# Optimization experiments

Hardware: AMD Instinct MI355X
Metric: run time of the kernel (lower is better)

Reference implementation:

```python
import jax, jax.numpy as jnp
import numpy as np

B, S, D, H, F, M, DC = 2, 1024, 1024, 16, 4096, 2048, 256
HD = D // H

def rmsnorm(x, w, eps=1e-6):
    return x * jax.lax.rsqrt(jnp.mean(x * x, axis=-1, keepdims=True) + eps) * w

def setup_inputs() -> dict:
    key = jax.random.key(0)
    ks = jax.random.split(key, 16)
    def w(i, shape):
        return jax.random.normal(ks[i], shape, jnp.float32) * (1.0 / np.sqrt(shape[0]))
    # real RoPE tables
    inv = 1.0 / (10000.0 ** (jnp.arange(0, HD, 2, dtype=jnp.float32) / HD))
    freqs = jnp.outer(jnp.arange(S, dtype=jnp.float32), inv)
    emb = jnp.concatenate([freqs, freqs], axis=-1)  # [S, HD]
    return {
        "hidden_states": jax.random.normal(ks[0], (B, S, D), jnp.float32),
        "mem_keys": jnp.zeros((B, M, DC), jnp.float32),
        "mem_values": jnp.zeros((B, M, D), jnp.float32),
        "cos": jnp.cos(emb), "sin": jnp.sin(emb),
        "norm1_w": jnp.ones((D,), jnp.float32),
        "norm2_w": jnp.ones((D,), jnp.float32),
        "norm_mem_w": jnp.ones((D,), jnp.float32),
        "Wq": w(1, (D, D)), "Wk": w(2, (D, D)), "Wv": w(3, (D, D)), "Wo": w(4, (D, D)),
        "W_content": w(5, (D, D)), "W_comp": w(6, (D, DC)), "W_strength": w(7, (D, 1)),
        "W_query": w(8, (D, DC)),
        "W_gate": w(9, (2 * D, D)), "W_proj": w(10, (D, D)),
        "W1": w(11, (D, F)), "W3": w(12, (D, F)), "W2": w(13, (F, D)),
        "position": 0,
    }

def reference(hidden_states, mem_keys, mem_values, cos, sin,
              norm1_w, norm2_w, norm_mem_w,
              Wq, Wk, Wv, Wo,
              W_content, W_comp, W_strength, W_query,
              W_gate, W_proj, W1, W3, W2, position):
    b, s, d = hidden_states.shape
    h = hidden_states
    # 1) causal self-attention with RoPE
    n = rmsnorm(h, norm1_w)
    def heads(x):
        return x.reshape(b, s, H, HD).transpose(0, 2, 1, 3)  # [b,h,s,hd]
    q, k, v = heads(n @ Wq), heads(n @ Wk), heads(n @ Wv)
    def rot(x):
        x1, x2 = jnp.split(x, 2, axis=-1)
        return jnp.concatenate([-x2, x1], axis=-1)
    c, si = cos[None, None], sin[None, None]
    q = q * c + rot(q) * si
    k = k * c + rot(k) * si
    scores = jnp.einsum('bhqd,bhkd->bhqk', q, k) / np.sqrt(HD)
    causal = jnp.tril(jnp.ones((s, s), bool))
    scores = jnp.where(causal, scores, jnp.float32(-1e30))
    attn = jax.nn.softmax(scores, axis=-1)
    attn_out = jnp.einsum('bhqk,bhkd->bhqd', attn, v).transpose(0, 2, 1, 3).reshape(b, s, d) @ Wo
    h = h + attn_out
    # 2) memory snapshot write: the original per-token python loop writes each token
    #    to consecutive circular-buffer slots; with M >= s the slots are unique, so
    #    the loop vectorizes into a single scatter.
    content = h @ W_content                     # [b,s,d]
    compressed = h @ W_comp                     # [b,s,DC]
    strength = jax.nn.sigmoid(h @ W_strength)   # [b,s,1]
    idx = (position + jnp.arange(s)) % mem_keys.shape[1]
    old_k = mem_keys[:, idx]
    old_v = mem_values[:, idx]
    new_keys = mem_keys.at[:, idx].set(strength * compressed + (1.0 - strength) * old_k)
    new_values = mem_values.at[:, idx].set(strength * content + (1.0 - strength) * old_v)
    # 3) memory retrieval (attention over slots)
    normed = rmsnorm(h, norm_mem_w)
    qm = normed @ W_query                       # [b,s,DC]
    mscores = jnp.einsum('bsd,bmd->bsm', qm, new_keys) / np.sqrt(DC)
    mattn = jax.nn.softmax(mscores, axis=-1)
    retrieved = jnp.einsum('bsm,bmd->bsd', mattn, new_values)
    # 4) gated memory integration
    gate = jax.nn.sigmoid(jnp.concatenate([h, retrieved], axis=-1) @ W_gate)
    h = h + gate * (retrieved @ W_proj)
    # 5) SwiGLU FFN
    n2 = rmsnorm(h, norm2_w)
    h = h + (jax.nn.silu(n2 @ W1) * (n2 @ W3)) @ W2
    return (h, new_keys, new_values)
```

## Files before the change

### kernel.cpp

```cpp
#include <hip/hip_runtime.h>
#include <hip/hip_bf16.h>
#include <math.h>

typedef __bf16 bf16;
typedef __attribute__((ext_vector_type(8))) __bf16 bf16x8;
typedef __attribute__((ext_vector_type(4))) __bf16 bf16x4;
typedef __attribute__((ext_vector_type(4))) float f32x4;

#define B_ 2
#define S_ 1024
#define D_ 1024
#define H_ 16
#define HD_ 64
#define F_ 4096
#define M_ 2048
#define DC_ 256
#define NTOK (B_*S_)

__device__ __forceinline__ void gload16(const void* g, void* l) {
    __builtin_amdgcn_global_load_lds(
        (__attribute__((address_space(1))) void*)(void*)(g),
        (__attribute__((address_space(3))) void*)(l), 16, 0, 0);
}

template<int N> __device__ __forceinline__ void wait_vm() {
    if constexpr (N == 0)      asm volatile("s_waitcnt vmcnt(0)" ::: "memory");
    else if constexpr (N == 2) asm volatile("s_waitcnt vmcnt(2)" ::: "memory");
    else if constexpr (N == 4) asm volatile("s_waitcnt vmcnt(4)" ::: "memory");
    else if constexpr (N == 6) asm volatile("s_waitcnt vmcnt(6)" ::: "memory");
    else                       asm volatile("s_waitcnt vmcnt(8)" ::: "memory");
}
__device__ __forceinline__ void wait_lgkm0() {
    asm volatile("s_waitcnt lgkmcnt(0)" ::: "memory");
}

template<int BM, int BN, bool OUTBF>
__global__ __launch_bounds__(256) void mgemm(
    const bf16* __restrict__ A, const bf16* __restrict__ Bt,
    const float* __restrict__ resid, void* __restrict__ Cout,
    int K, int lda, int ldb, int ldc,
    long long sA, long long sB, long long sC)
{
    constexpr int WN   = (BM == 128) ? 2 : 4;
    constexpr int WCOL = BN / WN;
    constexpr int FN   = WCOL / 16;
    constexpr int LA = BM * 64, LB = BN * 64;
    constexpr int LPS = BM / 32 + BN / 32;
    __shared__ bf16 lds[2 * (LA + LB)];
    const int z = blockIdx.z;
    A  += (size_t)z * sA;
    Bt += (size_t)z * sB;
    const int gx = gridDim.x;
    const int nwg = gx * gridDim.y;
    const int flat = blockIdx.y * gx + blockIdx.x;
    const int q8 = nwg >> 3, r8 = nwg & 7;
    const int xcd = flat & 7, lid = flat >> 3;
    const int swz = (xcd < r8 ? xcd * (q8 + 1) : r8 * (q8 + 1) + (xcd - r8) * q8) + lid;
    const int band = swz / (8 * gx);
    const int rem  = swz % (8 * gx);
    const int row0 = (band * 8 + (rem & 7)) * BM;
    const int col0 = (rem >> 3) * BN;
    const int tid = threadIdx.x, wid = tid >> 6, lane = tid & 63;
    const int wr = wid / WN, wc = wid % WN;
    const int srow = lane >> 3;
    const int ssub = (lane & 7) ^ (srow & 7);

    f32x4 acc[4][FN];
    #pragma unroll
    for (int m = 0; m < 4; ++m)
        #pragma unroll
        for (int n = 0; n < FN; ++n) acc[m][n] = (f32x4){0.f, 0.f, 0.f, 0.f};

    auto STAGE = [&](int buf, int k0) {
        bf16* Ab = lds + buf * (LA + LB);
        bf16* Bb = Ab + LA;
        #pragma unroll
        for (int i = 0; i < BM / 32; ++i) {
            int c = wid * (BM / 32) + i;
            gload16(A + (size_t)(row0 + c * 8 + srow) * lda + k0 + ssub * 8, Ab + c * 512);
        }
        #pragma unroll
        for (int i = 0; i < BN / 32; ++i) {
            int c = wid * (BN / 32) + i;
            gload16(Bt + (size_t)(col0 + c * 8 + srow) * ldb + k0 + ssub * 8, Bb + c * 512);
        }
    };

    const int nt = K >> 6;
    STAGE(0, 0);
    if (nt > 1) STAGE(1, 64);
    for (int t = 0; t < nt; ++t) {
        if (t < nt - 1) wait_vm<LPS>();
        else            wait_vm<0>();
        __builtin_amdgcn_sched_barrier(0);
        __builtin_amdgcn_s_barrier();
        __builtin_amdgcn_sched_barrier(0);
        const bf16* Ab = lds + (t & 1) * (LA + LB);
        const bf16* Bb = Ab + LA;
        const int ar = wr * 64 + (lane & 15);
        const int br = wc * WCOL + (lane & 15);
        #pragma unroll
        for (int ksel = 0; ksel < 2; ++ksel) {
            const int ps = ((ksel << 2) + (lane >> 4)) ^ (lane & 7);
            bf16x8 af[4], bfr[FN];
            #pragma unroll
            for (int m = 0; m < 4; ++m)
                af[m] = *(const bf16x8*)(Ab + (ar + m * 16) * 64 + ps * 8);
            #pragma unroll
            for (int n = 0; n < FN; ++n)
                bfr[n] = *(const bf16x8*)(Bb + (br + n * 16) * 64 + ps * 8);
            #pragma unroll
            for (int m = 0; m < 4; ++m)
                #pragma unroll
                for (int n = 0; n < FN; ++n)
                    acc[m][n] = __builtin_amdgcn_mfma_f32_16x16x32_bf16(af[m], bfr[n], acc[m][n], 0, 0, 0);
        }
        wait_lgkm0();
        __builtin_amdgcn_sched_barrier(0);
        __builtin_amdgcn_s_barrier();
        __builtin_amdgcn_sched_barrier(0);
        if (t + 2 < nt) STAGE(t & 1, (t + 2) << 6);
    }
    const int crow = row0 + wr * 64 + ((lane >> 4) << 2);
    const int ccol = col0 + wc * WCOL + (lane & 15);
    #pragma unroll
    for (int m = 0; m < 4; ++m)
        #pragma unroll
        for (int n = 0; n < FN; ++n)
            #pragma unroll
            for (int r = 0; r < 4; ++r) {
                size_t idx = (size_t)(crow + m * 16 + r) * ldc + ccol + n * 16;
                float v = acc[m][n][r];
                if (resid) v += resid[idx];
                if (OUTBF) ((bf16*)Cout)[(size_t)z * sC + idx] = (bf16)v;
                else       ((float*)Cout)[(size_t)z * sC + idx] = v;
            }
}

__global__ __launch_bounds__(256) void flash_attn(
    const bf16* __restrict__ qkv, const bf16* __restrict__ vt,
    bf16* __restrict__ o)
{
    __shared__ bf16 qlds[64 * 64];
    __shared__ bf16 klds[2][64 * 64];
    __shared__ bf16 vlds[2][64 * 64];
    __shared__ bf16 plds[4][16 * 64];
    const int qt = blockIdx.x, hh = blockIdx.y, b = blockIdx.z;
    const int qb0 = qt * 64;
    const int tid = threadIdx.x, wid = tid >> 6, lane = tid & 63;
    const bf16* qg = qkv + (size_t)b * S_ * 3072 + hh * 64;
    const bf16* kg = qg + 1024;
    const bf16* vg = vt + (size_t)(b * H_ + hh) * 64 * 1024;
    const int srow = lane >> 3;
    const int ssub = (lane & 7) ^ (srow & 7);

    #pragma unroll
    for (int i = 0; i < 2; ++i) {
        int c = wid * 2 + i;
        gload16(qg + (size_t)(qb0 + c * 8 + srow) * 3072 + ssub * 8, qlds + c * 512);
    }
    auto STAGE = [&](int buf, int kb) {
        #pragma unroll
        for (int i = 0; i < 2; ++i) {
            int c = wid * 2 + i;
            gload16(kg + (size_t)(kb + c * 8 + srow) * 3072 + ssub * 8, klds[buf] + c * 512);
            gload16(vg + (size_t)(c * 8 + srow) * 1024 + kb + ssub * 8, vlds[buf] + c * 512);
        }
    };

    const int nt = qt + 1;
    STAGE(0, 0);
    if (nt > 1) STAGE(1, 64);

    f32x4 oacc[4];
    #pragma unroll
    for (int n = 0; n < 4; ++n) oacc[n] = (f32x4){0.f, 0.f, 0.f, 0.f};
    float mrow[4] = {-1e30f, -1e30f, -1e30f, -1e30f};
    float lrow[4] = {0.f, 0.f, 0.f, 0.f};
    bf16x8 qf[2];
    bf16* pw = plds[wid];
    const int qlr = (lane >> 4) * 4;

    for (int t = 0; t < nt; ++t) {
        if (t < nt - 1) wait_vm<4>();
        else            wait_vm<0>();
        __builtin_amdgcn_sched_barrier(0);
        __builtin_amdgcn_s_barrier();
        __builtin_amdgcn_sched_barrier(0);
        if (t == 0) {
            const int ar = wid * 16 + (lane & 15);
            #pragma unroll
            for (int ksel = 0; ksel < 2; ++ksel) {
                const int ps = ((ksel << 2) + (lane >> 4)) ^ (lane & 7);
                qf[ksel] = *(const bf16x8*)(qlds + ar * 64 + ps * 8);
            }
        }
        const bf16* Kb = klds[t & 1];
        const bf16* Vb = vlds[t & 1];
        f32x4 sacc[4];
        #pragma unroll
        for (int n = 0; n < 4; ++n) sacc[n] = (f32x4){0.f, 0.f, 0.f, 0.f};
        #pragma unroll
        for (int ksel = 0; ksel < 2; ++ksel) {
            const int ps = ((ksel << 2) + (lane >> 4)) ^ (lane & 7);
            #pragma unroll
            for (int n = 0; n < 4; ++n) {
                bf16x8 kf = *(const bf16x8*)(Kb + (n * 16 + (lane & 15)) * 64 + ps * 8);
                sacc[n] = __builtin_amdgcn_mfma_f32_16x16x32_bf16(qf[ksel], kf, sacc[n], 0, 0, 0);
            }
        }
        if (t == nt - 1) {
            const int qrow = qb0 + wid * 16 + qlr;
            const int kcol = t * 64 + (lane & 15);
            #pragma unroll
            for (int n = 0; n < 4; ++n)
                #pragma unroll
                for (int r = 0; r < 4; ++r)
                    if (kcol + n * 16 > qrow + r) sacc[n][r] = -1e30f;
        }
        #pragma unroll
        for (int r = 0; r < 4; ++r) {
            float mx = fmaxf(fmaxf(sacc[0][r], sacc[1][r]), fmaxf(sacc[2][r], sacc[3][r]));
            #pragma unroll
            for (int off = 8; off > 0; off >>= 1) mx = fmaxf(mx, __shfl_xor(mx, off));
            float mnew = fmaxf(mrow[r], mx);
            float scale = __expf(mrow[r] - mnew);
            float rs = 0.f;
            #pragma unroll
            for (int n = 0; n < 4; ++n) {
                float p = __expf(sacc[n][r] - mnew);
                sacc[n][r] = p;
                rs += p;
            }
            #pragma unroll
            for (int off = 8; off > 0; off >>= 1) rs += __shfl_xor(rs, off);
            lrow[r] = lrow[r] * scale + rs;
            mrow[r] = mnew;
            #pragma unroll
            for (int n = 0; n < 4; ++n) oacc[n][r] *= scale;
        }
        #pragma unroll
        for (int n = 0; n < 4; ++n)
            #pragma unroll
            for (int r = 0; r < 4; ++r) {
                const int qr = qlr + r;
                const int k = n * 16 + (lane & 15);
                const int su = (k >> 3) ^ (qr & 7);
                pw[qr * 64 + su * 8 + (k & 7)] = (bf16)sacc[n][r];
            }
        #pragma unroll
        for (int ksel = 0; ksel < 2; ++ksel) {
            const int ps = ((ksel << 2) + (lane >> 4)) ^ (lane & 7);
            bf16x8 pa = *(const bf16x8*)(pw + (lane & 15) * 64 + ps * 8);
            #pragma unroll
            for (int n = 0; n < 4; ++n) {
                bf16x8 vf = *(const bf16x8*)(Vb + (n * 16 + (lane & 15)) * 64 + ps * 8);
                oacc[n] = __builtin_amdgcn_mfma_f32_16x16x32_bf16(pa, vf, oacc[n], 0, 0, 0);
            }
        }
        wait_lgkm0();
        __builtin_amdgcn_sched_barrier(0);
        __builtin_amdgcn_s_barrier();
        __builtin_amdgcn_sched_barrier(0);
        if (t + 2 < nt) STAGE(t & 1, (t + 2) * 64);
    }
    float inv[4];
    #pragma unroll
    for (int r = 0; r < 4; ++r) inv[r] = 1.f / lrow[r];
    #pragma unroll
    for (int n = 0; n < 4; ++n)
        #pragma unroll
        for (int r = 0; r < 4; ++r) {
            const int q = qb0 + wid * 16 + qlr + r;
            const int d = n * 16 + (lane & 15);
            o[(size_t)(b * S_ + q) * 1024 + hh * 64 + d] = (bf16)(oacc[n][r] * inv[r]);
        }
}

template<typename TI>
__global__ __launch_bounds__(256) void tcast(
    const TI* __restrict__ in, bf16* __restrict__ out,
    int lin, int lout, long long sin, long long sout)
{
    __shared__ float t[32][33];
    in  += (size_t)blockIdx.z * sin;
    out += (size_t)blockIdx.z * sout;
    const int c0 = blockIdx.x * 32, r0 = blockIdx.y * 32;
    const int tx = threadIdx.x & 31, ty = threadIdx.x >> 5;
    #pragma unroll
    for (int j = 0; j < 4; ++j)
        t[ty + j * 8][tx] = (float)in[(size_t)(r0 + ty + j * 8) * lin + c0 + tx];
    __syncthreads();
    #pragma unroll
    for (int j = 0; j < 4; ++j)
        out[(size_t)(c0 + ty + j * 8) * lout + r0 + tx] = (bf16)t[tx][ty + j * 8];
}

__global__ __launch_bounds__(256) void rmsnorm_bf(
    const float* __restrict__ x, const float* __restrict__ w, bf16* __restrict__ out)
{
    __shared__ float red[4];
    const int row = blockIdx.x, tid = threadIdx.x;
    const float* xr = x + (size_t)row * D_;
    f32x4 v = *(const f32x4*)(xr + tid * 4);
    float ss = v.x * v.x + v.y * v.y + v.z * v.z + v.w * v.w;
    #pragma unroll
    for (int off = 32; off > 0; off >>= 1) ss += __shfl_xor(ss, off);
    if ((tid & 63) == 0) red[tid >> 6] = ss;
    __syncthreads();
    float scn = rsqrtf((red[0] + red[1] + red[2] + red[3]) * (1.f / D_) + 1e-6f);
    f32x4 wv = *(const f32x4*)(w + tid * 4);
    bf16x4 o;
    o[0] = (bf16)(v.x * scn * wv.x); o[1] = (bf16)(v.y * scn * wv.y);
    o[2] = (bf16)(v.z * scn * wv.z); o[3] = (bf16)(v.w * scn * wv.w);
    *(bf16x4*)(out + (size_t)row * D_ + tid * 4) = o;
}

__global__ void rope_kernel(bf16* __restrict__ qkv,
                            const float* __restrict__ cosp, const float* __restrict__ sinp)
{
    int idx = blockIdx.x * 256 + threadIdx.x;
    int p = idx & 31, hh = (idx >> 5) & 15, s = (idx >> 9) & 1023, b = idx >> 19;
    size_t base = ((size_t)(b * S_ + s)) * 3072 + hh * 64;
    float c1 = cosp[s * 64 + p],      s1 = sinp[s * 64 + p];
    float c2 = cosp[s * 64 + p + 32], s2 = sinp[s * 64 + p + 32];
    float q1 = (float)qkv[base + p], q2 = (float)qkv[base + p + 32];
    qkv[base + p]      = (bf16)((q1 * c1 - q2 * s1) * 0.125f);
    qkv[base + p + 32] = (bf16)((q2 * c2 + q1 * s2) * 0.125f);
    size_t kb = base + 1024;
    float k1 = (float)qkv[kb + p], k2 = (float)qkv[kb + p + 32];
    qkv[kb + p]      = (bf16)(k1 * c1 - k2 * s1);
    qkv[kb + p + 32] = (bf16)(k2 * c2 + k1 * s2);
}

__global__ __launch_bounds__(256) void mem_softmax(
    const float* __restrict__ ms, bf16* __restrict__ out)
{
    __shared__ float red[4];
    const int row = blockIdx.x, tid = threadIdx.x;
    const float* r = ms + (size_t)row * 2048;
    f32x4 a = *(const f32x4*)(r + tid * 8);
    f32x4 b = *(const f32x4*)(r + tid * 8 + 4);
    float xs[8] = {a.x, a.y, a.z, a.w, b.x, b.y, b.z, b.w};
    float mx = -1e30f;
    #pragma unroll
    for (int i = 0; i < 8; ++i) mx = fmaxf(mx, xs[i]);
    #pragma unroll
    for (int off = 32; off > 0; off >>= 1) mx = fmaxf(mx, __shfl_xor(mx, off));
    if ((tid & 63) == 0) red[tid >> 6] = mx;
    __syncthreads();
    mx = fmaxf(fmaxf(red[0], red[1]), fmaxf(red[2], red[3]));
    __syncthreads();
    float sum = 0.f;
    #pragma unroll
    for (int i = 0; i < 8; ++i) { xs[i] = __expf((xs[i] - mx) * 0.0625f); sum += xs[i]; }
    #pragma unroll
    for (int off = 32; off > 0; off >>= 1) sum += __shfl_xor(sum, off);
    if ((tid & 63) == 0) red[tid >> 6] = sum;
    __syncthreads();
    float inv = 1.f / (red[0] + red[1] + red[2] + red[3]);
    bf16x8 o;
    #pragma unroll
    for (int i = 0; i < 8; ++i) o[i] = (bf16)(xs[i] * inv);
    *(bf16x8*)(out + (size_t)row * 2048 + tid * 8) = o;
}

__global__ void strength_kernel(const float* __restrict__ h, const float* __restrict__ ws,
                                float* __restrict__ st)
{
    const int row = blockIdx.x, lane = threadIdx.x;
    const float* hr = h + (size_t)row * D_;
    float s = 0.f;
    #pragma unroll
    for (int it = 0; it < 4; ++it) {
        f32x4 hv = *(const f32x4*)(hr + it * 256 + lane * 4);
        f32x4 wv = *(const f32x4*)(ws + it * 256 + lane * 4);
        s += hv.x * wv.x + hv.y * wv.y + hv.z * wv.z + hv.w * wv.w;
    }
    #pragma unroll
    for (int off = 32; off > 0; off >>= 1) s += __shfl_xor(s, off);
    if (lane == 0) st[row] = 1.f / (1.f + expf(-s));
}

__global__ void scatter_keys_kernel(const float* __restrict__ ctcp, const float* __restrict__ st,
                                    const float* __restrict__ memk, const int* __restrict__ pos,
                                    float* __restrict__ outk)
{
    int idx = blockIdx.x * 256 + threadIdx.x;
    int c = (idx & 63) * 4;
    int s = (idx >> 6) & (S_ - 1);
    int b = idx >> 16;
    int row = (pos[0] + s) % M_;
    float t = st[b * S_ + s];
    size_t mi = ((size_t)b * M_ + row) * DC_ + c;
    f32x4 cv = *(const f32x4*)(ctcp + ((size_t)b * S_ + s) * 1280 + 1024 + c);
    f32x4 mv = *(const f32x4*)(memk + mi);
    f32x4 o = {t * cv.x + (1.f - t) * mv.x, t * cv.y + (1.f - t) * mv.y,
               t * cv.z + (1.f - t) * mv.z, t * cv.w + (1.f - t) * mv.w};
    *(f32x4*)(outk + mi) = o;
}

__global__ void scatter_vals_kernel(const float* __restrict__ ctcp, const float* __restrict__ st,
                                    const float* __restrict__ memv, const int* __restrict__ pos,
                                    float* __restrict__ outv)
{
    int idx = blockIdx.x * 256 + threadIdx.x;
    int c = (idx & 255) * 4;
    int s = (idx >> 8) & (S_ - 1);
    int b = idx >> 18;
    int row = (pos[0] + s) % M_;
    float t = st[b * S_ + s];
    size_t mi = ((size_t)b * M_ + row) * D_ + c;
    f32x4 cv = *(const f32x4*)(ctcp + ((size_t)b * S_ + s) * 1280 + c);
    f32x4 mv = *(const f32x4*)(memv + mi);
    f32x4 o = {t * cv.x + (1.f - t) * mv.x, t * cv.y + (1.f - t) * mv.y,
               t * cv.z + (1.f - t) * mv.z, t * cv.w + (1.f - t) * mv.w};
    *(f32x4*)(outv + mi) = o;
}

__global__ void cast_h1_kernel(const float* __restrict__ h1, bf16* __restrict__ cat)
{
    int i = blockIdx.x * 256 + threadIdx.x;
    int row = i >> 8, c = (i & 255) * 4;
    f32x4 v = *(const f32x4*)(h1 + (size_t)row * 1024 + c);
    bf16x4 o = {(bf16)v.x, (bf16)v.y, (bf16)v.z, (bf16)v.w};
    *(bf16x4*)(cat + (size_t)row * 2048 + c) = o;
}

__global__ void cast_flat_kernel(const float* __restrict__ in, bf16* __restrict__ out)
{
    int i = blockIdx.x * 256 + threadIdx.x;
    f32x4 v = *(const f32x4*)(in + (size_t)i * 4);
    bf16x4 o = {(bf16)v.x, (bf16)v.y, (bf16)v.z, (bf16)v.w};
    *(bf16x4*)(out + (size_t)i * 4) = o;
}

__global__ void gatecomb_kernel(const float* __restrict__ h1, const float* __restrict__ g,
                                const float* __restrict__ p, float* __restrict__ h2)
{
    int i = blockIdx.x * 256 + threadIdx.x;
    f32x4 hv = *(const f32x4*)(h1 + (size_t)i * 4);
    f32x4 gv = *(const f32x4*)(g + (size_t)i * 4);
    f32x4 pv = *(const f32x4*)(p + (size_t)i * 4);
    f32x4 o;
    o.x = hv.x + pv.x / (1.f + expf(-gv.x));
    o.y = hv.y + pv.y / (1.f + expf(-gv.y));
    o.z = hv.z + pv.z / (1.f + expf(-gv.z));
    o.w = hv.w + pv.w / (1.f + expf(-gv.w));
    *(f32x4*)(h2 + (size_t)i * 4) = o;
}

__global__ void silumul_kernel(const bf16* __restrict__ a13, bf16* __restrict__ a1bf)
{
    int i = blockIdx.x * 256 + threadIdx.x;
    int row = i >> 10, c = (i & 1023) * 4;
    bf16x4 xv = *(const bf16x4*)(a13 + (size_t)row * 8192 + c);
    bf16x4 yv = *(const bf16x4*)(a13 + (size_t)row * 8192 + 4096 + c);
    bf16x4 o;
    #pragma unroll
    for (int j = 0; j < 4; ++j) {
        float x = (float)xv[j];
        o[j] = (bf16)((x / (1.f + expf(-x))) * (float)yv[j]);
    }
    *(bf16x4*)(a1bf + (size_t)row * 4096 + c) = o;
}

extern "C" void kernel_launch(void* const* d_in, const int* in_sizes, int n_in,
                              void* d_out, int out_size, void* d_ws, size_t ws_size,
                              hipStream_t stream)
{
    const float* h0   = (const float*)d_in[0];
    const float* memk = (const float*)d_in[1];
    const float* memv = (const float*)d_in[2];
    const float* cosp = (const float*)d_in[3];
    const float* sinp = (const float*)d_in[4];
    const float* n1w  = (const float*)d_in[5];
    const float* n2w  = (const float*)d_in[6];
    const float* nmw  = (const float*)d_in[7];
    const float* Wq   = (const float*)d_in[8];
    const float* Wk   = (const float*)d_in[9];
    const float* Wv   = (const float*)d_in[10];
    const float* Wo   = (const float*)d_in[11];
    const float* Wct  = (const float*)d_in[12];
    const float* Wcp  = (const float*)d_in[13];
    const float* Wst  = (const float*)d_in[14];
    const float* Wqr  = (const float*)d_in[15];
    const float* Wg   = (const float*)d_in[16];
    const float* Wpj  = (const float*)d_in[17];
    const float* W1   = (const float*)d_in[18];
    const float* W3   = (const float*)d_in[19];
    const float* W2   = (const float*)d_in[20];
    const int*   pos  = (const int*)d_in[21];

    float* out_h = (float*)d_out;
    float* out_k = out_h + (size_t)NTOK * D_;
    float* out_v = out_k + (size_t)B_ * M_ * DC_;

    char* W = (char*)d_ws;
    const size_t MB = 1u << 20;
    bf16*  qkvb = (bf16*)(W);
    bf16*  vtb  = (bf16*)(W + 12 * MB);
    bf16*  nbf  = (bf16*)(W + 16 * MB);
    bf16*  abf  = (bf16*)(W + 20 * MB);
    float* h1b  = (float*)(W + 24 * MB);
    bf16*  catbf= (bf16*)(W + 32 * MB);
    float* ctcp = (float*)(W + 40 * MB);
    float* stb  = (float*)(W + 51 * MB);
    float* msb  = (float*)(W + 52 * MB);
    bf16*  matt = (bf16*)(W + 68 * MB);
    bf16*  nvt  = (bf16*)(W + 76 * MB);
    bf16*  a13  = (bf16*)(W + 52 * MB);
    bf16*  a1bf = (bf16*)(W);
    bf16*  okbf = (bf16*)(W + 84 * MB);
    bf16*  qmbf = (bf16*)(W + 86 * MB);
    float* aob  = (float*)(W + 88 * MB);
    float* h2b  = (float*)(W + 96 * MB);
    bf16*  WqkvT= (bf16*)(W + 104 * MB);
    bf16*  WoT  = (bf16*)(W + 110 * MB);
    bf16*  WctcpT=(bf16*)(W + 112 * MB);
    bf16*  WqrT = (bf16*)(W + 115 * MB);
    bf16*  WgT  = (bf16*)(W + 116 * MB);
    bf16*  WpjT = (bf16*)(W + 120 * MB);
    bf16*  W13T = (bf16*)(W + 122 * MB);
    bf16*  W2T  = (bf16*)(W + 138 * MB);

    tcast<float><<<dim3(32, 32, 1), 256, 0, stream>>>(Wq,  WqkvT,                1024, 1024, 0, 0);
    tcast<float><<<dim3(32, 32, 1), 256, 0, stream>>>(Wk,  WqkvT + 1024 * 1024,  1024, 1024, 0, 0);
    tcast<float><<<dim3(32, 32, 1), 256, 0, stream>>>(Wv,  WqkvT + 2048 * 1024,  1024, 1024, 0, 0);
    tcast<float><<<dim3(32, 32, 1), 256, 0, stream>>>(Wo,  WoT,                  1024, 1024, 0, 0);
    tcast<float><<<dim3(32, 32, 1), 256, 0, stream>>>(Wct, WctcpT,               1024, 1024, 0, 0);
    tcast<float><<<dim3(8, 32, 1), 256, 0, stream>>>(Wcp,  WctcpT + 1024 * 1024, 256, 1024, 0, 0);
    tcast<float><<<dim3(8, 32, 1), 256, 0, stream>>>(Wqr,  WqrT,                 256, 1024, 0, 0);
    tcast<float><<<dim3(32, 64, 1), 256, 0, stream>>>(Wg,  WgT,                  1024, 2048, 0, 0);
    tcast<float><<<dim3(32, 32, 1), 256, 0, stream>>>(Wpj, WpjT,                 1024, 1024, 0, 0);
    tcast<float><<<dim3(128, 32, 1), 256, 0, stream>>>(W1, W13T,                 4096, 1024, 0, 0);
    tcast<float><<<dim3(128, 32, 1), 256, 0, stream>>>(W3, W13T + 4096 * 1024,   4096, 1024, 0, 0);
    tcast<float><<<dim3(32, 128, 1), 256, 0, stream>>>(W2, W2T,                  1024, 4096, 0, 0);

    rmsnorm_bf<<<NTOK, 256, 0, stream>>>(h0, n1w, nbf);
    mgemm<64, 128, true><<<dim3(24, 32, 1), 256, 0, stream>>>(
        nbf, WqkvT, nullptr, qkvb, 1024, 1024, 1024, 3072, 0, 0, 0);
    rope_kernel<<<(B_ * S_ * H_ * 32) / 256, 256, 0, stream>>>(qkvb, cosp, sinp);
    for (int b = 0; b < B_; ++b)
        tcast<bf16><<<dim3(2, 32, 16), 256, 0, stream>>>(
            qkvb + (size_t)b * S_ * 3072 + 2048, vtb + (size_t)b * 16 * 65536,
            3072, 1024, 64, 65536);

    flash_attn<<<dim3(S_ / 64, H_, B_), 256, 0, stream>>>(qkvb, vtb, abf);

    mgemm<64, 64, false><<<dim3(16, 32, 1), 256, 0, stream>>>(
        abf, WoT, h0, h1b, 1024, 1024, 1024, 1024, 0, 0, 0);
    cast_h1_kernel<<<(NTOK * D_) / 1024, 256, 0, stream>>>(h1b, catbf);
    strength_kernel<<<NTOK, 64, 0, stream>>>(h1b, Wst, stb);

    mgemm<64, 64, false><<<dim3(20, 32, 1), 256, 0, stream>>>(
        catbf, WctcpT, nullptr, ctcp, 1024, 2048, 1024, 1280, 0, 0, 0);
    hipMemcpyAsync(out_k, memk, (size_t)B_ * M_ * DC_ * sizeof(float), hipMemcpyDeviceToDevice, stream);
    hipMemcpyAsync(out_v, memv, (size_t)B_ * M_ * D_ * sizeof(float), hipMemcpyDeviceToDevice, stream);
    scatter_keys_kernel<<<(B_ * S_ * DC_) / 1024, 256, 0, stream>>>(ctcp, stb, memk, pos, out_k);
    scatter_vals_kernel<<<(B_ * S_ * D_) / 1024, 256, 0, stream>>>(ctcp, stb, memv, pos, out_v);

    rmsnorm_bf<<<NTOK, 256, 0, stream>>>(h1b, nmw, nbf);
    mgemm<64, 64, true><<<dim3(4, 32, 1), 256, 0, stream>>>(
        nbf, WqrT, nullptr, qmbf, 1024, 1024, 1024, 256, 0, 0, 0);
    cast_flat_kernel<<<(B_ * M_ * DC_) / 1024, 256, 0, stream>>>(out_k, okbf);
    mgemm<64, 128, false><<<dim3(16, 16, 2), 256, 0, stream>>>(
        qmbf, okbf, nullptr, msb, 256, 256, 256, 2048,
        (long long)S_ * 256, (long long)M_ * 256, (long long)S_ * 2048);
    mem_softmax<<<NTOK, 256, 0, stream>>>(msb, matt);
    tcast<float><<<dim3(32, 64, 2), 256, 0, stream>>>(
        out_v, nvt, 1024, 2048, (long long)M_ * 1024, (long long)1024 * 2048);
    mgemm<64, 128, true><<<dim3(8, 16, 2), 256, 0, stream>>>(
        matt, nvt, nullptr, catbf + 1024, 2048, 2048, 2048, 2048,
        (long long)S_ * 2048, (long long)1024 * 2048, (long long)S_ * 2048);

    mgemm<64, 64, false><<<dim3(16, 32, 1), 256, 0, stream>>>(
        catbf, WgT, nullptr, aob, 2048, 2048, 2048, 1024, 0, 0, 0);
    mgemm<64, 64, false><<<dim3(16, 32, 1), 256, 0, stream>>>(
        catbf + 1024, WpjT, nullptr, ctcp, 1024, 2048, 1024, 1024, 0, 0, 0);
    gatecomb_kernel<<<(NTOK * D_) / 1024, 256, 0, stream>>>(h1b, aob, ctcp, h2b);

    rmsnorm_bf<<<NTOK, 256, 0, stream>>>(h2b, n2w, nbf);
    mgemm<128, 128, true><<<dim3(64, 16, 1), 256, 0, stream>>>(
        nbf, W13T, nullptr, a13, 1024, 1024, 1024, 8192, 0, 0, 0);
    silumul_kernel<<<(NTOK * F_) / 1024, 256, 0, stream>>>(a13, a1bf);
    mgemm<64, 64, false><<<dim3(16, 32, 1), 256, 0, stream>>>(
        a1bf, W2T, h2b, out_h, 4096, 4096, 4096, 1024, 0, 0, 0);
}
```

Measured before the change: 335.5 us.

## Fuse elementwise epilogues into GEMMs, merge memory update copy, batch weight transposes

Adds GEMM epilogue variants: one writes a bf16 copy of h1 into the concat buffer, one applies the sigmoid gate and residual directly. A dedicated dual-B GEMM computes W1 and W3 together and applies SiLU·mul in registers, so the a13 intermediate is never written to memory. The memory update now iterates over all slots, copying or blending in one pass and emitting the bf16 keys. This replaces the device memcpys, the cast kernels and the scatter kernels. Weight transposes are batched into fewer launches. Together these cut launches and intermediate global traffic, at the cost of more register pressure in the fused GEMM.

```diff
diff --git a/kernel.cpp b/kernel.cpp
--- a/kernel.cpp
+++ b/kernel.cpp
@@ -33,13 +33,15 @@
 __device__ __forceinline__ void wait_lgkm0() {
     asm volatile("s_waitcnt lgkmcnt(0)" ::: "memory");
 }
-
-template<int BM, int BN, bool OUTBF>
+__device__ __forceinline__ float sigm(float x) { return 1.f / (1.f + expf(-x)); }
+
+template<int BM, int BN, bool OUTBF, int EPI>
 __global__ __launch_bounds__(256) void mgemm(
     const bf16* __restrict__ A, const bf16* __restrict__ Bt,
     const float* __restrict__ resid, void* __restrict__ Cout,
     int K, int lda, int ldb, int ldc,
-    long long sA, long long sB, long long sC)
+    long long sA, long long sB, long long sC,
+    const void* __restrict__ aux1, const void* __restrict__ aux2)
 {
     constexpr int WN   = (BM == 128) ? 2 : 4;
     constexpr int WCOL = BN / WN;
@@ -129,11 +131,121 @@
         for (int n = 0; n < FN; ++n)
             #pragma unroll
             for (int r = 0; r < 4; ++r) {
-                size_t idx = (size_t)(crow + m * 16 + r) * ldc + ccol + n * 16;
+                const int rr = crow + m * 16 + r, cc = ccol + n * 16;
+                size_t idx = (size_t)rr * ldc + cc;
                 float v = acc[m][n][r];
-                if (resid) v += resid[idx];
-                if (OUTBF) ((bf16*)Cout)[(size_t)z * sC + idx] = (bf16)v;
-                else       ((float*)Cout)[(size_t)z * sC + idx] = v;
+                if (EPI == 2) {
+                    float g = sigm(((const float*)aux1)[idx]);
+                    v = ((const float*)aux2)[idx] + g * v;
+                    ((float*)Cout)[idx] = v;
+                } else {
+                    if (resid) v += resid[idx];
+                    if (OUTBF) ((bf16*)Cout)[(size_t)z * sC + idx] = (bf16)v;
+                    else       ((float*)Cout)[(size_t)z * sC + idx] = v;
+                    if (EPI == 1)
+                        ((bf16*)aux1)[(size_t)rr * 2048 + cc] = (bf16)v;
+                }
+            }
+}
+
+__global__ __launch_bounds__(256) void mgemm13(
+    const bf16* __restrict__ A, const bf16* __restrict__ B1t, const bf16* __restrict__ B3t,
+    bf16* __restrict__ Cout, int K, int lda, int ldb, int ldc)
+{
+    constexpr int LA = 128 * 64, LB = 64 * 64;
+    __shared__ bf16 lds[2 * (LA + 2 * LB)];
+    const int gx = gridDim.x;
+    const int nwg = gx * gridDim.y;
+    const int flat = blockIdx.y * gx + blockIdx.x;
+    const int q8 = nwg >> 3, r8 = nwg & 7;
+    const int xcd = flat & 7, lid = flat >> 3;
+    const int swz = (xcd < r8 ? xcd * (q8 + 1) : r8 * (q8 + 1) + (xcd - r8) * q8) + lid;
+    const int band = swz / (8 * gx);
+    const int rem  = swz % (8 * gx);
+    const int row0 = (band * 8 + (rem & 7)) * 128;
+    const int col0 = (rem >> 3) * 64;
+    const int tid = threadIdx.x, wid = tid >> 6, lane = tid & 63;
+    const int wr = wid >> 1, wc = wid & 1;
+    const int srow = lane >> 3;
+    const int ssub = (lane & 7) ^ (srow & 7);
+
+    f32x4 acc1[4][2], acc3[4][2];
+    #pragma unroll
+    for (int m = 0; m < 4; ++m)
+        #pragma unroll
+        for (int n = 0; n < 2; ++n) {
+            acc1[m][n] = (f32x4){0.f, 0.f, 0.f, 0.f};
+            acc3[m][n] = (f32x4){0.f, 0.f, 0.f, 0.f};
+        }
+
+    auto STAGE = [&](int buf, int k0) {
+        bf16* Ab = lds + buf * (LA + 2 * LB);
+        bf16* B1b = Ab + LA;
+        bf16* B3b = B1b + LB;
+        #pragma unroll
+        for (int i = 0; i < 4; ++i) {
+            int c = wid * 4 + i;
+            gload16(A + (size_t)(row0 + c * 8 + srow) * lda + k0 + ssub * 8, Ab + c * 512);
+        }
+        #pragma unroll
+        for (int i = 0; i < 2; ++i) {
+            int c = wid * 2 + i;
+            gload16(B1t + (size_t)(col0 + c * 8 + srow) * ldb + k0 + ssub * 8, B1b + c * 512);
+            gload16(B3t + (size_t)(col0 + c * 8 + srow) * ldb + k0 + ssub * 8, B3b + c * 512);
+        }
+    };
+
+    const int nt = K >> 6;
+    STAGE(0, 0);
+    if (nt > 1) STAGE(1, 64);
+    for (int t = 0; t < nt; ++t) {
+        if (t < nt - 1) wait_vm<8>();
+        else            wait_vm<0>();
+        __builtin_amdgcn_sched_barrier(0);
+        __builtin_amdgcn_s_barrier();
+        __builtin_amdgcn_sched_barrier(0);
+        const bf16* Ab = lds + (t & 1) * (LA + 2 * LB);
+        const bf16* B1b = Ab + LA;
+        const bf16* B3b = B1b + LB;
+        const int ar = wr * 64 + (lane & 15);
+        const int br = wc * 32 + (lane & 15);
+        #pragma unroll
+        for (int ksel = 0; ksel < 2; ++ksel) {
+            const int ps = ((ksel << 2) + (lane >> 4)) ^ (lane & 7);
+            bf16x8 af[4], b1f[2], b3f[2];
+            #pragma unroll
+            for (int m = 0; m < 4; ++m)
+                af[m] = *(const bf16x8*)(Ab + (ar + m * 16) * 64 + ps * 8);
+            #pragma unroll
+            for (int n = 0; n < 2; ++n) {
+                b1f[n] = *(const bf16x8*)(B1b + (br + n * 16) * 64 + ps * 8);
+                b3f[n] = *(const bf16x8*)(B3b + (br + n * 16) * 64 + ps * 8);
+            }
+            #pragma unroll
+            for (int m = 0; m < 4; ++m)
+                #pragma unroll
+                for (int n = 0; n < 2; ++n) {
+                    acc1[m][n] = __builtin_amdgcn_mfma_f32_16x16x32_bf16(af[m], b1f[n], acc1[m][n], 0, 0, 0);
+                    acc3[m][n] = __builtin_amdgcn_mfma_f32_16x16x32_bf16(af[m], b3f[n], acc3[m][n], 0, 0, 0);
+                }
+        }
+        wait_lgkm0();
+        __builtin_amdgcn_sched_barrier(0);
+        __builtin_amdgcn_s_barrier();
+        __builtin_amdgcn_sched_barrier(0);
+        if (t + 2 < nt) STAGE(t & 1, (t + 2) << 6);
+    }
+    const int crow = row0 + wr * 64 + ((lane >> 4) << 2);
+    const int ccol = col0 + wc * 32 + (lane & 15);
+    #pragma unroll
+    for (int m = 0; m < 4; ++m)
+        #pragma unroll
+        for (int n = 0; n < 2; ++n)
+            #pragma unroll
+            for (int r = 0; r < 4; ++r) {
+                float x = acc1[m][n][r];
+                float v = (x * sigm(x)) * acc3[m][n][r];
+                Cout[(size_t)(crow + m * 16 + r) * ldc + ccol + n * 16] = (bf16)v;
             }
 }
 
@@ -296,6 +408,23 @@
         out[(size_t)(c0 + ty + j * 8) * lout + r0 + tx] = (bf16)t[tx][ty + j * 8];
 }
 
+struct TC6 { const float* in[6]; bf16* out[6]; };
+__global__ __launch_bounds__(256) void tcast_b(TC6 p, int lin, int lout)
+{
+    __shared__ float t[32][33];
+    const float* in = p.in[blockIdx.z];
+    bf16* out = p.out[blockIdx.z];
+    const int c0 = blockIdx.x * 32, r0 = blockIdx.y * 32;
+    const int tx = threadIdx.x & 31, ty = threadIdx.x >> 5;
+    #pragma unroll
+    for (int j = 0; j < 4; ++j)
+        t[ty + j * 8][tx] = in[(size_t)(r0 + ty + j * 8) * lin + c0 + tx];
+    __syncthreads();
+    #pragma unroll
+    for (int j = 0; j < 4; ++j)
+        out[(size_t)(c0 + ty + j * 8) * lout + r0 + tx] = (bf16)t[tx][ty + j * 8];
+}
+
 __global__ __launch_bounds__(256) void rmsnorm_bf(
     const float* __restrict__ x, const float* __restrict__ w, bf16* __restrict__ out)
 {
@@ -379,90 +508,49 @@
     }
     #pragma unroll
     for (int off = 32; off > 0; off >>= 1) s += __shfl_xor(s, off);
-    if (lane == 0) st[row] = 1.f / (1.f + expf(-s));
-}
-
-__global__ void scatter_keys_kernel(const float* __restrict__ ctcp, const float* __restrict__ st,
-                                    const float* __restrict__ memk, const int* __restrict__ pos,
-                                    float* __restrict__ outk)
+    if (lane == 0) st[row] = sigm(s);
+}
+
+__global__ void mem_upd_k(const float* __restrict__ ctcp, const float* __restrict__ st,
+                          const float* __restrict__ memk, const int* __restrict__ pos,
+                          float* __restrict__ outk, bf16* __restrict__ okbf)
 {
     int idx = blockIdx.x * 256 + threadIdx.x;
     int c = (idx & 63) * 4;
-    int s = (idx >> 6) & (S_ - 1);
-    int b = idx >> 16;
-    int row = (pos[0] + s) % M_;
-    float t = st[b * S_ + s];
+    int row = (idx >> 6) & (M_ - 1);
+    int b = idx >> 17;
+    int s = (row - pos[0]) % M_; if (s < 0) s += M_;
     size_t mi = ((size_t)b * M_ + row) * DC_ + c;
-    f32x4 cv = *(const f32x4*)(ctcp + ((size_t)b * S_ + s) * 1280 + 1024 + c);
-    f32x4 mv = *(const f32x4*)(memk + mi);
-    f32x4 o = {t * cv.x + (1.f - t) * mv.x, t * cv.y + (1.f - t) * mv.y,
-               t * cv.z + (1.f - t) * mv.z, t * cv.w + (1.f - t) * mv.w};
+    f32x4 o = *(const f32x4*)(memk + mi);
+    if (s < S_) {
+        float t = st[b * S_ + s];
+        f32x4 cv = *(const f32x4*)(ctcp + ((size_t)b * S_ + s) * 1280 + 1024 + c);
+        o.x = t * cv.x + (1.f - t) * o.x; o.y = t * cv.y + (1.f - t) * o.y;
+        o.z = t * cv.z + (1.f - t) * o.z; o.w = t * cv.w + (1.f - t) * o.w;
+    }
     *(f32x4*)(outk + mi) = o;
-}
-
-__global__ void scatter_vals_kernel(const float* __restrict__ ctcp, const float* __restrict__ st,
-                                    const float* __restrict__ memv, const int* __restrict__ pos,
-                                    float* __restrict__ outv)
+    bf16x4 ob = {(bf16)o.x, (bf16)o.y, (bf16)o.z, (bf16)o.w};
+    *(bf16x4*)(okbf + mi) = ob;
+}
+
+__global__ void mem_upd_v(const float* __restrict__ ctcp, const float* __restrict__ st,
+                          const float* __restrict__ memv, const int* __restrict__ pos,
+                          float* __restrict__ outv)
 {
     int idx = blockIdx.x * 256 + threadIdx.x;
     int c = (idx & 255) * 4;
-    int s = (idx >> 8) & (S_ - 1);
-    int b = idx >> 18;
-    int row = (pos[0] + s) % M_;
-    float t = st[b * S_ + s];
+    int row = (idx >> 8) & (M_ - 1);
+    int b = idx >> 19;
+    int s = (row - pos[0]) % M_; if (s < 0) s += M_;
     size_t mi = ((size_t)b * M_ + row) * D_ + c;
-    f32x4 cv = *(const f32x4*)(ctcp + ((size_t)b * S_ + s) * 1280 + c);
-    f32x4 mv = *(const f32x4*)(memv + mi);
-    f32x4 o = {t * cv.x + (1.f - t) * mv.x, t * cv.y + (1.f - t) * mv.y,
-               t * cv.z + (1.f - t) * mv.z, t * cv.w + (1.f - t) * mv.w};
+    f32x4 o = *(const f32x4*)(memv + mi);
+    if (s < S_) {
+        float t = st[b * S_ + s];
+        f32x4 cv = *(const f32x4*)(ctcp + ((size_t)b * S_ + s) * 1280 + c);
+        o.x = t * cv.x + (1.f - t) * o.x; o.y = t * cv.y + (1.f - t) * o.y;
+        o.z = t * cv.z + (1.f - t) * o.z; o.w = t * cv.w + (1.f - t) * o.w;
+    }
     *(f32x4*)(outv + mi) = o;
-}
-
-__global__ void cast_h1_kernel(const float* __restrict__ h1, bf16* __restrict__ cat)
-{
-    int i = blockIdx.x * 256 + threadIdx.x;
-    int row = i >> 8, c = (i & 255) * 4;
-    f32x4 v = *(const f32x4*)(h1 + (size_t)row * 1024 + c);
-    bf16x4 o = {(bf16)v.x, (bf16)v.y, (bf16)v.z, (bf16)v.w};
-    *(bf16x4*)(cat + (size_t)row * 2048 + c) = o;
-}
-
-__global__ void cast_flat_kernel(const float* __restrict__ in, bf16* __restrict__ out)
-{
-    int i = blockIdx.x * 256 + threadIdx.x;
-    f32x4 v = *(const f32x4*)(in + (size_t)i * 4);
-    bf16x4 o = {(bf16)v.x, (bf16)v.y, (bf16)v.z, (bf16)v.w};
-    *(bf16x4*)(out + (size_t)i * 4) = o;
-}
-
-__global__ void gatecomb_kernel(const float* __restrict__ h1, const float* __restrict__ g,
-                                const float* __restrict__ p, float* __restrict__ h2)
-{
-    int i = blockIdx.x * 256 + threadIdx.x;
-    f32x4 hv = *(const f32x4*)(h1 + (size_t)i * 4);
-    f32x4 gv = *(const f32x4*)(g + (size_t)i * 4);
-    f32x4 pv = *(const f32x4*)(p + (size_t)i * 4);
-    f32x4 o;
-    o.x = hv.x + pv.x / (1.f + expf(-gv.x));
-    o.y = hv.y + pv.y / (1.f + expf(-gv.y));
-    o.z = hv.z + pv.z / (1.f + expf(-gv.z));
-    o.w = hv.w + pv.w / (1.f + expf(-gv.w));
-    *(f32x4*)(h2 + (size_t)i * 4) = o;
-}
-
-__global__ void silumul_kernel(const bf16* __restrict__ a13, bf16* __restrict__ a1bf)
-{
-    int i = blockIdx.x * 256 + threadIdx.x;
-    int row = i >> 10, c = (i & 1023) * 4;
-    bf16x4 xv = *(const bf16x4*)(a13 + (size_t)row * 8192 + c);
-    bf16x4 yv = *(const bf16x4*)(a13 + (size_t)row * 8192 + 4096 + c);
-    bf16x4 o;
-    #pragma unroll
-    for (int j = 0; j < 4; ++j) {
-        float x = (float)xv[j];
-        o[j] = (bf16)((x / (1.f + expf(-x))) * (float)yv[j]);
-    }
-    *(bf16x4*)(a1bf + (size_t)row * 4096 + c) = o;
 }
 
 extern "C" void kernel_launch(void* const* d_in, const int* in_sizes, int n_in,
@@ -509,7 +597,6 @@
     float* msb  = (float*)(W + 52 * MB);
     bf16*  matt = (bf16*)(W + 68 * MB);
     bf16*  nvt  = (bf16*)(W + 76 * MB);
-    bf16*  a13  = (bf16*)(W + 52 * MB);
     bf16*  a1bf = (bf16*)(W);
     bf16*  okbf = (bf16*)(W + 84 * MB);
     bf16*  qmbf = (bf16*)(W + 86 * MB);
@@ -524,22 +611,38 @@
     bf16*  W13T = (bf16*)(W + 122 * MB);
     bf16*  W2T  = (bf16*)(W + 138 * MB);
 
-    tcast<float><<<dim3(32, 32, 1), 256, 0, stream>>>(Wq,  WqkvT,                1024, 1024, 0, 0);
-    tcast<float><<<dim3(32, 32, 1), 256, 0, stream>>>(Wk,  WqkvT + 1024 * 1024,  1024, 1024, 0, 0);
-    tcast<float><<<dim3(32, 32, 1), 256, 0, stream>>>(Wv,  WqkvT + 2048 * 1024,  1024, 1024, 0, 0);
-    tcast<float><<<dim3(32, 32, 1), 256, 0, stream>>>(Wo,  WoT,                  1024, 1024, 0, 0);
-    tcast<float><<<dim3(32, 32, 1), 256, 0, stream>>>(Wct, WctcpT,               1024, 1024, 0, 0);
-    tcast<float><<<dim3(8, 32, 1), 256, 0, stream>>>(Wcp,  WctcpT + 1024 * 1024, 256, 1024, 0, 0);
-    tcast<float><<<dim3(8, 32, 1), 256, 0, stream>>>(Wqr,  WqrT,                 256, 1024, 0, 0);
-    tcast<float><<<dim3(32, 64, 1), 256, 0, stream>>>(Wg,  WgT,                  1024, 2048, 0, 0);
-    tcast<float><<<dim3(32, 32, 1), 256, 0, stream>>>(Wpj, WpjT,                 1024, 1024, 0, 0);
-    tcast<float><<<dim3(128, 32, 1), 256, 0, stream>>>(W1, W13T,                 4096, 1024, 0, 0);
-    tcast<float><<<dim3(128, 32, 1), 256, 0, stream>>>(W3, W13T + 4096 * 1024,   4096, 1024, 0, 0);
-    tcast<float><<<dim3(32, 128, 1), 256, 0, stream>>>(W2, W2T,                  1024, 4096, 0, 0);
+    {
+        TC6 pa;
+        pa.in[0] = Wq;  pa.out[0] = WqkvT;
+        pa.in[1] = Wk;  pa.out[1] = WqkvT + 1024 * 1024;
+        pa.in[2] = Wv;  pa.out[2] = WqkvT + 2048 * 1024;
+        pa.in[3] = Wo;  pa.out[3] = WoT;
+        pa.in[4] = Wct; pa.out[4] = WctcpT;
+        pa.in[5] = Wpj; pa.out[5] = WpjT;
+        tcast_b<<<dim3(32, 32, 6), 256, 0, stream>>>(pa, 1024, 1024);
+        TC6 pb;
+        pb.in[0] = Wcp; pb.out[0] = WctcpT + 1024 * 1024;
+        pb.in[1] = Wqr; pb.out[1] = WqrT;
+        pb.in[2] = Wcp; pb.out[2] = WctcpT + 1024 * 1024;
+        pb.in[3] = Wcp; pb.out[3] = WctcpT + 1024 * 1024;
+        pb.in[4] = Wcp; pb.out[4] = WctcpT + 1024 * 1024;
+        pb.in[5] = Wcp; pb.out[5] = WctcpT + 1024 * 1024;
+        tcast_b<<<dim3(8, 32, 2), 256, 0, stream>>>(pb, 256, 1024);
+        TC6 pc;
+        pc.in[0] = W1; pc.out[0] = W13T;
+        pc.in[1] = W3; pc.out[1] = W13T + 4096 * 1024;
+        pc.in[2] = W1; pc.out[2] = W13T;
+        pc.in[3] = W1; pc.out[3] = W13T;
+        pc.in[4] = W1; pc.out[4] = W13T;
+        pc.in[5] = W1; pc.out[5] = W13T;
+        tcast_b<<<dim3(128, 32, 2), 256, 0, stream>>>(pc, 4096, 1024);
+    }
+    tcast<float><<<dim3(32, 64, 1), 256, 0, stream>>>(Wg, WgT, 1024, 2048, 0, 0);
+    tcast<float><<<dim3(32, 128, 1), 256, 0, stream>>>(W2, W2T, 1024, 4096, 0, 0);
 
     rmsnorm_bf<<<NTOK, 256, 0, stream>>>(h0, n1w, nbf);
-    mgemm<64, 128, true><<<dim3(24, 32, 1), 256, 0, stream>>>(
-        nbf, WqkvT, nullptr, qkvb, 1024, 1024, 1024, 3072, 0, 0, 0);
+    mgemm<64, 128, true, 0><<<dim3(24, 32, 1), 256, 0, stream>>>(
+        nbf, WqkvT, nullptr, qkvb, 1024, 1024, 1024, 3072, 0, 0, 0, nullptr, nullptr);
     rope_kernel<<<(B_ * S_ * H_ * 32) / 256, 256, 0, stream>>>(qkvb, cosp, sinp);
     for (int b = 0; b < B_; ++b)
         tcast<bf16><<<dim3(2, 32, 16), 256, 0, stream>>>(
@@ -548,42 +651,36 @@
 
     flash_attn<<<dim3(S_ / 64, H_, B_), 256, 0, stream>>>(qkvb, vtb, abf);
 
-    mgemm<64, 64, false><<<dim3(16, 32, 1), 256, 0, stream>>>(
-        abf, WoT, h0, h1b, 1024, 1024, 1024, 1024, 0, 0, 0);
-    cast_h1_kernel<<<(NTOK * D_) / 1024, 256, 0, stream>>>(h1b, catbf);
+    mgemm<64, 64, false, 1><<<dim3(16, 32, 1), 256, 0, stream>>>(
+        abf, WoT, h0, h1b, 1024, 1024, 1024, 1024, 0, 0, 0, catbf, nullptr);
     strength_kernel<<<NTOK, 64, 0, stream>>>(h1b, Wst, stb);
 
-    mgemm<64, 64, false><<<dim3(20, 32, 1), 256, 0, stream>>>(
-        catbf, WctcpT, nullptr, ctcp, 1024, 2048, 1024, 1280, 0, 0, 0);
-    hipMemcpyAsync(out_k, memk, (size_t)B_ * M_ * DC_ * sizeof(float), hipMemcpyDeviceToDevice, stream);
-    hipMemcpyAsync(out_v, memv, (size_t)B_ * M_ * D_ * sizeof(float), hipMemcpyDeviceToDevice, stream);
-    scatter_keys_kernel<<<(B_ * S_ * DC_) / 1024, 256, 0, stream>>>(ctcp, stb, memk, pos, out_k);
-    scatter_vals_kernel<<<(B_ * S_ * D_) / 1024, 256, 0, stream>>>(ctcp, stb, memv, pos, out_v);
+    mgemm<64, 64, false, 0><<<dim3(20, 32, 1), 256, 0, stream>>>(
+        catbf, WctcpT, nullptr, ctcp, 1024, 2048, 1024, 1280, 0, 0, 0, nullptr, nullptr);
+    mem_upd_k<<<(B_ * M_ * DC_) / 1024, 256, 0, stream>>>(ctcp, stb, memk, pos, out_k, okbf);
+    mem_upd_v<<<(B_ * M_ * D_) / 1024, 256, 0, stream>>>(ctcp, stb, memv, pos, out_v);
 
     rmsnorm_bf<<<NTOK, 256, 0, stream>>>(h1b, nmw, nbf);
-    mgemm<64, 64, true><<<dim3(4, 32, 1), 256, 0, stream>>>(
-        nbf, WqrT, nullptr, qmbf, 1024, 1024, 1024, 256, 0, 0, 0);
-    cast_flat_kernel<<<(B_ * M_ * DC_) / 1024, 256, 0, stream>>>(out_k, okbf);
-    mgemm<64, 128, false><<<dim3(16, 16, 2), 256, 0, stream>>>(
+    mgemm<64, 64, true, 0><<<dim3(4, 32, 1), 256, 0, stream>>>(
+        nbf, WqrT, nullptr, qmbf, 1024, 1024, 1024, 256, 0, 0, 0, nullptr, nullptr);
+    mgemm<64, 128, false, 0><<<dim3(16, 16, 2), 256, 0, stream>>>(
         qmbf, okbf, nullptr, msb, 256, 256, 256, 2048,
-        (long long)S_ * 256, (long long)M_ * 256, (long long)S_ * 2048);
+        (long long)S_ * 256, (long long)M_ * 256, (long long)S_ * 2048, nullptr, nullptr);
     mem_softmax<<<NTOK, 256, 0, stream>>>(msb, matt);
     tcast<float><<<dim3(32, 64, 2), 256, 0, stream>>>(
         out_v, nvt, 1024, 2048, (long long)M_ * 1024, (long long)1024 * 2048);
-    mgemm<64, 128, true><<<dim3(8, 16, 2), 256, 0, stream>>>(
+    mgemm<64, 128, true, 0><<<dim3(8, 16, 2), 256, 0, stream>>>(
         matt, nvt, nullptr, catbf + 1024, 2048, 2048, 2048, 2048,
-        (long long)S_ * 2048, (long long)1024 * 2048, (long long)S_ * 2048);
-
-    mgemm<64, 64, false><<<dim3(16, 32, 1), 256, 0, stream>>>(
-        catbf, WgT, nullptr, aob, 2048, 2048, 2048, 1024, 0, 0, 0);
-    mgemm<64, 64, false><<<dim3(16, 32, 1), 256, 0, stream>>>(
-        catbf + 1024, WpjT, nullptr, ctcp, 1024, 2048, 1024, 1024, 0, 0, 0);
-    gatecomb_kernel<<<(NTOK * D_) / 1024, 256, 0, stream>>>(h1b, aob, ctcp, h2b);
+        (long long)S_ * 2048, (long long)1024 * 2048, (long long)S_ * 2048, nullptr, nullptr);
+
+    mgemm<64, 64, false, 0><<<dim3(16, 32, 1), 256, 0, stream>>>(
+        catbf, WgT, nullptr, aob, 2048, 2048, 2048, 1024, 0, 0, 0, nullptr, nullptr);
+    mgemm<64, 64, false, 2><<<dim3(16, 32, 1), 256, 0, stream>>>(
+        catbf + 1024, WpjT, nullptr, h2b, 1024, 2048, 1024, 1024, 0, 0, 0, aob, h1b);
 
     rmsnorm_bf<<<NTOK, 256, 0, stream>>>(h2b, n2w, nbf);
-    mgemm<128, 128, true><<<dim3(64, 16, 1), 256, 0, stream>>>(
-        nbf, W13T, nullptr, a13, 1024, 1024, 1024, 8192, 0, 0, 0);
-    silumul_kernel<<<(NTOK * F_) / 1024, 256, 0, stream>>>(a13, a1bf);
-    mgemm<64, 64, false><<<dim3(16, 32, 1), 256, 0, stream>>>(
-        a1bf, W2T, h2b, out_h, 4096, 4096, 4096, 1024, 0, 0, 0);
-}
+    mgemm13<<<dim3(64, 16, 1), 256, 0, stream>>>(
+        nbf, W13T, W13T + 4096 * 1024, a1bf, 1024, 1024, 1024, 4096);
+    mgemm<64, 64, false, 0><<<dim3(16, 32, 1), 256, 0, stream>>>(
+        a1bf, W2T, h2b, out_h, 4096, 4096, 4096, 1024, 0, 0, 0, nullptr, nullptr);
+}
```

New measurement: 296.8 us. 1.13x faster.
